# Kernel optimization log

Measured on AMD Instinct MI355X. Metric: run time of the kernel, lower is better.

Reference implementation:

```python
import jax, jax.numpy as jnp
import numpy as np

NPOINT, K = 1024, 16
BN_EPS = 1e-5


def farthest_point_sample(xyz, npoint):
    # xyz: [B, N, 3]. Deterministic start at index 0 (torch version uses randint).
    B, N, _ = xyz.shape

    def step(carry, _):
        distance, farthest = carry
        centroid = jnp.take_along_axis(xyz, farthest[:, None, None], axis=1)  # [B,1,3]
        dist = jnp.sum((xyz - centroid) ** 2, axis=-1)  # [B,N]
        distance = jnp.minimum(distance, dist)
        nxt = jnp.argmax(distance, axis=-1)
        return (distance, nxt), farthest

    init = (jnp.full((B, N), 1e10, dtype=xyz.dtype), jnp.zeros((B,), dtype=jnp.int32))
    _, cents = jax.lax.scan(step, init, None, length=npoint)
    return jnp.transpose(cents)  # [B, npoint]


def knn_idx(k, xyz, new_xyz):
    # squared distances [B,S,N] via ||a||^2 + ||b||^2 - 2 a.b (avoids [B,S,N,3] blowup)
    d = (jnp.sum(new_xyz ** 2, -1)[:, :, None]
         + jnp.sum(xyz ** 2, -1)[:, None, :]
         - 2.0 * jnp.einsum('bsc,bnc->bsn', new_xyz, xyz))
    _, idx = jax.lax.top_k(-d, k)  # k smallest distances
    return idx


def gather_points(points, idx):
    # points: [B,N,C], idx: [B,...] -> [B,...,C]
    return jax.vmap(lambda p, i: p[i])(points, idx)


def bn_train(x, gamma, beta):
    # BatchNorm1d in train mode: batch statistics, biased variance
    m = jnp.mean(x, axis=0)
    v = jnp.var(x, axis=0)
    return gamma * (x - m) * jax.lax.rsqrt(v + BN_EPS) + beta


def setup_inputs() -> dict:
    key = jax.random.key(0)
    ks = jax.random.split(key, 16)
    B, N, CIN, COUT = 8, 4096, 64, 128
    cin3 = CIN + 3          # 67
    ec = int(cin3 * 2.0)    # 134 (expand_ratio=2, hidden_ch arg is unused by InvResMLP)
    s = 0.05
    return {
        'xyz': jax.random.normal(ks[0], (B, N, 3), jnp.float32),
        'pts': jax.random.normal(ks[1], (B, N, CIN), jnp.float32),
        'fc1_w': jax.random.normal(ks[2], (cin3, ec), jnp.float32) * s,
        'fc1_b': jnp.zeros((ec,), jnp.float32),
        'bn1_g': jnp.ones((ec,), jnp.float32),
        'bn1_b': jnp.zeros((ec,), jnp.float32),
        'fc2_w': jax.random.normal(ks[3], (ec, ec), jnp.float32) * s,
        'fc2_b': jnp.zeros((ec,), jnp.float32),
        'bn2_g': jnp.ones((ec,), jnp.float32),
        'bn2_b': jnp.zeros((ec,), jnp.float32),
        'fc3_w': jax.random.normal(ks[4], (ec, COUT), jnp.float32) * s,
        'fc3_b': jnp.zeros((COUT,), jnp.float32),
        'bn3_g': jnp.ones((COUT,), jnp.float32),
        'bn3_b': jnp.zeros((COUT,), jnp.float32),
        'sc_w': jax.random.normal(ks[5], (cin3, COUT), jnp.float32) * s,
        'sc_b': jnp.zeros((COUT,), jnp.float32),
        'scbn_g': jnp.ones((COUT,), jnp.float32),
        'scbn_b': jnp.zeros((COUT,), jnp.float32),
    }


def reference(xyz, pts, fc1_w, fc1_b, bn1_g, bn1_b, fc2_w, fc2_b, bn2_g, bn2_b,
              fc3_w, fc3_b, bn3_g, bn3_b, sc_w, sc_b, scbn_g, scbn_b):
    # --- local_group: FPS + kNN grouping ---
    cent = farthest_point_sample(xyz, NPOINT)          # [B,S]
    new_xyz = gather_points(xyz, cent)                 # [B,S,3]
    idx = knn_idx(K, xyz, new_xyz)                     # [B,S,K]
    grouped_xyz = gather_points(xyz, idx)              # [B,S,K,3]
    grouped_pts = gather_points(pts, idx)              # [B,S,K,C]
    grouped_xyz_norm = grouped_xyz - new_xyz[:, :, None, :]
    x = jnp.concatenate([grouped_xyz_norm, grouped_pts], axis=-1)  # [B,S,K,C+3]

    # --- InvResMLP (pointwise, train-mode BN, dropout as identity) ---
    B, S, Kk, C = x.shape
    x = x.reshape(B * S * Kk, C)
    sc = bn_train(x @ sc_w + sc_b, scbn_g, scbn_b)
    h = jax.nn.relu(bn_train(x @ fc1_w + fc1_b, bn1_g, bn1_b))
    h = jax.nn.relu(bn_train(h @ fc2_w + fc2_b, bn2_g, bn2_b))
    h = bn_train(h @ fc3_w + fc3_b, bn3_g, bn3_b)
    h = jax.nn.relu(h + sc)
    feats = h.reshape(B, S, Kk, -1)

    new_pts = jnp.max(feats, axis=2)                   # [B,S,out_ch]
    return new_xyz, new_pts
```

## Files before the change

### kernel.cpp

```cpp
#include <hip/hip_runtime.h>
#include <cstdint>
#include <cstddef>

typedef short short8 __attribute__((ext_vector_type(8)));
typedef float f32x4 __attribute__((ext_vector_type(4)));

#define B_   8
#define N_   4096
#define S_   1024
#define K_   16
#define M_   131072
#define CIN_ 64

__device__ inline float bf2f(unsigned short u) {
    unsigned int v = ((unsigned int)u) << 16;
    return __builtin_bit_cast(float, v);
}
__device__ inline unsigned short f2bf(float f) {
    unsigned int u = __builtin_bit_cast(unsigned int, f);
    unsigned int lsb = (u >> 16) & 1u;
    u += 0x7fffu + lsb;
    return (unsigned short)(u >> 16);
}

template<int CTRL>
__device__ inline unsigned long long dpp_max(unsigned long long k) {
    unsigned lo = (unsigned)k, hi = (unsigned)(k >> 32);
    unsigned olo = (unsigned)__builtin_amdgcn_update_dpp(0, (int)lo, CTRL, 0xF, 0xF, true);
    unsigned ohi = (unsigned)__builtin_amdgcn_update_dpp(0, (int)hi, CTRL, 0xF, 0xF, true);
    unsigned long long ok = ((unsigned long long)ohi << 32) | (unsigned long long)olo;
    return ok > k ? ok : k;
}
__device__ inline unsigned long long swz16_max(unsigned long long k) {
    unsigned lo = (unsigned)k, hi = (unsigned)(k >> 32);
    unsigned olo = (unsigned)__builtin_amdgcn_ds_swizzle((int)lo, 0x401F);
    unsigned ohi = (unsigned)__builtin_amdgcn_ds_swizzle((int)hi, 0x401F);
    unsigned long long ok = ((unsigned long long)ohi << 32) | (unsigned long long)olo;
    return ok > k ? ok : k;
}
__device__ inline unsigned long long shf32_max(unsigned long long k) {
    unsigned lo = (unsigned)k, hi = (unsigned)(k >> 32);
    unsigned olo = (unsigned)__shfl_xor((int)lo, 32);
    unsigned ohi = (unsigned)__shfl_xor((int)hi, 32);
    unsigned long long ok = ((unsigned long long)ohi << 32) | (unsigned long long)olo;
    return ok > k ? ok : k;
}

__global__ __launch_bounds__(256) void fps_kernel(const float* __restrict__ xyz,
                                                  float* __restrict__ outxyz)
{
    __shared__ float px_s[N_], py_s[N_], pz_s[N_];
    __shared__ float sOut[S_ * 3];
    __shared__ unsigned long long sK[2][4];
    int b = blockIdx.x;
    const float* xb = xyz + (size_t)b * N_ * 3;
    int t = threadIdx.x;
    int w = t >> 6, l = t & 63;
    const int NP = 16;
    float px[NP], py[NP], pz[NP], dst[NP];
#pragma unroll
    for (int i = 0; i < NP; i++) {
        int p = i * 256 + t;
        px[i] = xb[p * 3 + 0];
        py[i] = xb[p * 3 + 1];
        pz[i] = xb[p * 3 + 2];
        dst[i] = 1e10f;
        px_s[p] = px[i]; py_s[p] = py[i]; pz_s[p] = pz[i];
        asm volatile("" : "+v"(px[i]), "+v"(py[i]), "+v"(pz[i]));
    }
    __syncthreads();
    float cx = px_s[0], cy = py_s[0], cz = pz_s[0];
    for (int s = 0; s < S_; s++) {
        if (t == 0) { sOut[s * 3 + 0] = cx; sOut[s * 3 + 1] = cy; sOut[s * 3 + 2] = cz; }
        if (s == S_ - 1) break;
        float bd = -1.0f; int bp = 0;
#pragma unroll
        for (int i = 0; i < NP; i++) {
            float dx = __fsub_rn(px[i], cx);
            float dy = __fsub_rn(py[i], cy);
            float dz = __fsub_rn(pz[i], cz);
            float d  = __fadd_rn(__fadd_rn(__fmul_rn(dx, dx), __fmul_rn(dy, dy)),
                                 __fmul_rn(dz, dz));
            float nd = fminf(dst[i], d);
            dst[i] = nd;
            if (nd > bd) { bd = nd; bp = i * 256 + t; }
        }
        unsigned long long key =
            ((unsigned long long)__builtin_bit_cast(unsigned, bd) << 32) |
            (unsigned long long)(unsigned)(4095 - bp);
        key = dpp_max<0xB1>(key);
        key = dpp_max<0x4E>(key);
        key = dpp_max<0x141>(key);
        key = dpp_max<0x140>(key);
        key = swz16_max(key);
        key = shf32_max(key);
        int par = s & 1;
        if (l == 0) sK[par][w] = key;
        __syncthreads();
        unsigned long long k0 = sK[par][0], k1 = sK[par][1];
        unsigned long long k2 = sK[par][2], k3 = sK[par][3];
        unsigned long long ka = k0 > k1 ? k0 : k1;
        unsigned long long kb = k2 > k3 ? k2 : k3;
        unsigned long long g  = ka > kb ? ka : kb;
        int p = 4095 - (int)(g & 0xFFFu);
        cx = px_s[p]; cy = py_s[p]; cz = pz_s[p];
    }
    __syncthreads();
    float* ob = outxyz + (size_t)b * S_ * 3;
    for (int i = t; i < S_ * 3; i += 256) ob[i] = sOut[i];
}

__global__ void sqn_kernel(const float* __restrict__ xyz, float* __restrict__ sqn)
{
    int i = blockIdx.x * 256 + threadIdx.x;
    if (i >= B_ * N_) return;
    float x = xyz[i * 3 + 0], y = xyz[i * 3 + 1], z = xyz[i * 3 + 2];
    sqn[i] = __fadd_rn(__fadd_rn(__fmul_rn(x, x), __fmul_rn(y, y)), __fmul_rn(z, z));
}

__global__ __launch_bounds__(256) void knn_kernel(const float* __restrict__ xyz,
                                                  const float* __restrict__ sqn,
                                                  const float* __restrict__ newxyz,
                                                  int* __restrict__ idx)
{
    int w = threadIdx.x >> 6, l = threadIdx.x & 63;
    int q = blockIdx.x * 4 + w;
    int b = q >> 10;
    const float* xb = xyz + (size_t)b * N_ * 3;
    const float* sb = sqn + (size_t)b * N_;
    float qx = newxyz[(size_t)q * 3 + 0];
    float qy = newxyz[(size_t)q * 3 + 1];
    float qz = newxyz[(size_t)q * 3 + 2];
    float sa = __fadd_rn(__fadd_rn(__fmul_rn(qx, qx), __fmul_rn(qy, qy)), __fmul_rn(qz, qz));

    float d16[16]; int i16[16];
#pragma unroll
    for (int j = 0; j < 16; j++) { d16[j] = 3.0e38f; i16[j] = -1; }
    for (int i = 0; i < N_ / 64; i++) {
        int n = i * 64 + l;
        float bx = xb[n * 3 + 0], by = xb[n * 3 + 1], bz = xb[n * 3 + 2];
        float dot = __fmaf_rn(qz, bz, __fmaf_rn(qy, by, __fmul_rn(qx, bx)));
        float d = __fsub_rn(__fadd_rn(sa, sb[n]), __fmul_rn(2.0f, dot));
        if (d < d16[0]) {
            d16[0] = d; i16[0] = n;
#pragma unroll
            for (int j = 0; j < 15; j++) {
                if (d16[j] < d16[j + 1]) {
                    float td = d16[j]; d16[j] = d16[j + 1]; d16[j + 1] = td;
                    int   ti = i16[j]; i16[j] = i16[j + 1]; i16[j + 1] = ti;
                }
            }
        }
    }
    int* iq = idx + (size_t)q * 16;
#pragma unroll
    for (int r = 0; r < 16; r++) {
        float cd = d16[15]; int cn = i16[15];
#pragma unroll
        for (int off = 1; off < 64; off <<= 1) {
            float od = __shfl_xor(cd, off);
            int   on = __shfl_xor(cn, off);
            if (od < cd || (od == cd && on < cn)) { cd = od; cn = on; }
        }
        if (l == 0) iq[r] = cn;
        if (i16[15] == cn) {
#pragma unroll
            for (int j = 15; j >= 1; j--) { d16[j] = d16[j - 1]; i16[j] = i16[j - 1]; }
            d16[0] = 3.0e38f; i16[0] = -1;
        }
    }
}

__global__ void build_x(const float* __restrict__ xyz, const float* __restrict__ pts,
                        const float* __restrict__ newxyz, const int* __restrict__ idx,
                        unsigned short* __restrict__ X)
{
    size_t tid = (size_t)blockIdx.x * 256 + threadIdx.x;
    if (tid >= (size_t)M_ * 96) return;
    int c = (int)(tid % 96);
    size_t r = tid / 96;
    int s = (int)((r >> 4) & 1023);
    int b = (int)(r >> 14);
    int n = idx[r];
    float v;
    if (c < 3)      v = xyz[((size_t)b * N_ + n) * 3 + c] - newxyz[((size_t)b * S_ + s) * 3 + c];
    else if (c < 67) v = pts[((size_t)b * N_ + n) * CIN_ + (c - 3)];
    else             v = 0.0f;
    X[tid] = f2bf(v);
}

__global__ void fill_wt(unsigned short* __restrict__ dst, const float* __restrict__ src,
                        int Kreal, int Nrows, int Nsrc, int KPAD)
{
    int tid = blockIdx.x * 256 + threadIdx.x;
    if (tid >= Nrows * KPAD) return;
    int row = tid / KPAD, k = tid % KPAD;
    float v = (k < Kreal && row < Nsrc) ? src[(size_t)k * Nsrc + row] : 0.0f;
    dst[tid] = f2bf(v);
}

template<int KPAD, int NF>
__global__ __launch_bounds__(256) void gemm_bn(
    const unsigned short* __restrict__ A, const unsigned short* __restrict__ Wt,
    unsigned short* __restrict__ Z1, int ld1, int n1real, float* sum1, float* sq1,
    unsigned short* __restrict__ Z2, int ld2, int n2real, float* sum2, float* sq2,
    int split)
{
    __shared__ unsigned short sA[128 * KPAD];
    __shared__ float sSt[NF * 32];
    int t = threadIdx.x;
    int r0 = blockIdx.x * 128;
    for (int i = t; i < NF * 32; i += 256) sSt[i] = 0.0f;
    {
        const uint4* ga = (const uint4*)(A + (size_t)r0 * KPAD);
        uint4* la = (uint4*)sA;
        const int CNT = 128 * KPAD * 2 / 16;
        for (int i = t; i < CNT; i += 256) la[i] = ga[i];
    }
    __syncthreads();
    int w = t >> 6, l = t & 63, lhi = l >> 4, llo = l & 15;
    f32x4 acc[2][NF];
#pragma unroll
    for (int m = 0; m < 2; m++)
#pragma unroll
        for (int n = 0; n < NF; n++) acc[m][n] = (f32x4){0.f, 0.f, 0.f, 0.f};
#pragma unroll
    for (int ks = 0; ks < KPAD / 32; ks++) {
        short8 bfr[NF];
#pragma unroll
        for (int n = 0; n < NF; n++)
            bfr[n] = *(const short8*)(Wt + (size_t)(n * 16 + llo) * KPAD + ks * 32 + lhi * 8);
#pragma unroll
        for (int m = 0; m < 2; m++) {
            short8 afr = *(const short8*)(sA + (w * 32 + m * 16 + llo) * KPAD + ks * 32 + lhi * 8);
#pragma unroll
            for (int n = 0; n < NF; n++)
                acc[m][n] = __builtin_amdgcn_mfma_f32_16x16x32_bf16(afr, bfr[n], acc[m][n], 0, 0, 0);
        }
    }
#pragma unroll
    for (int n = 0; n < NF; n++) {
        int c = n * 16 + llo;
        float ss = 0.f, sq = 0.f;
#pragma unroll
        for (int m = 0; m < 2; m++) {
#pragma unroll
            for (int j = 0; j < 4; j++) {
                float v = acc[m][n][j];
                int row = r0 + w * 32 + m * 16 + lhi * 4 + j;
                unsigned short hv = f2bf(v);
                if (c < split) Z1[(size_t)row * ld1 + c] = hv;
                else           Z2[(size_t)row * ld2 + (c - split)] = hv;
                ss += v; sq += v * v;
            }
        }
        ss += __shfl_xor(ss, 16); ss += __shfl_xor(ss, 32);
        sq += __shfl_xor(sq, 16); sq += __shfl_xor(sq, 32);
        if (l < 16) { atomicAdd(&sSt[c * 2], ss); atomicAdd(&sSt[c * 2 + 1], sq); }
    }
    __syncthreads();
    for (int c = t; c < NF * 16; c += 256) {
        float ss = sSt[c * 2], sq = sSt[c * 2 + 1];
        if (c < split) {
            if (c < n1real) { atomicAdd(&sum1[c], ss); atomicAdd(&sq1[c], sq); }
        } else {
            int cc = c - split;
            if (cc < n2real) { atomicAdd(&sum2[cc], ss); atomicAdd(&sq2[cc], sq); }
        }
    }
}

__global__ void bn_finalize(const float* __restrict__ sum, const float* __restrict__ sq,
                            const float* __restrict__ g, const float* __restrict__ bb,
                            float* __restrict__ a, float* __restrict__ c, int n)
{
    int i = blockIdx.x * 256 + threadIdx.x;
    if (i >= n) return;
    const float inv = 1.0f / (float)M_;
    float m = sum[i] * inv;
    float var = sq[i] * inv - m * m;
    float av = g[i] * rsqrtf(var + 1e-5f);
    a[i] = av;
    c[i] = bb[i] - av * m;
}

__global__ void norm_relu(const unsigned short* __restrict__ Z, int zld, int nreal,
                          unsigned short* __restrict__ H, int hld,
                          const float* __restrict__ a, const float* __restrict__ c,
                          size_t total)
{
    size_t tid = (size_t)blockIdx.x * 256 + threadIdx.x;
    if (tid >= total) return;
    int col = (int)(tid % hld);
    size_t r = tid / hld;
    float v = 0.0f;
    if (col < nreal) v = fmaxf(a[col] * bf2f(Z[r * zld + col]) + c[col], 0.0f);
    H[r * hld + col] = f2bf(v);
}

__global__ void final_kernel(const unsigned short* __restrict__ Z3,
                             const unsigned short* __restrict__ ZSC,
                             const float* __restrict__ a3, const float* __restrict__ c3,
                             const float* __restrict__ asc, const float* __restrict__ csc,
                             float* __restrict__ out)
{
    int tid = blockIdx.x * 256 + threadIdx.x;
    int ch = tid & 127, bs = tid >> 7;
    float A3 = a3[ch], C3 = c3[ch], AS = asc[ch], CS = csc[ch];
    float mx = 0.0f;
    for (int k = 0; k < 16; k++) {
        size_t row = (size_t)bs * 16 + k;
        float v3 = bf2f(Z3[row * 128 + ch]);
        float vs = bf2f(ZSC[row * 128 + ch]);
        float y = fmaxf(A3 * v3 + C3 + AS * vs + CS, 0.0f);
        mx = fmaxf(mx, y);
    }
    out[24576 + (size_t)bs * 128 + ch] = mx;
}

#define WS_STATS 0
#define WS_WT1   16384
#define WS_WT2   68608
#define WS_WT3   114688
#define WS_SQN   155648
#define WS_IDX   286720
#define WS_X     811008
#define WS_Z     25976832
#define WS_ZSC   63725568
#define WS_H     97280000

extern "C" void kernel_launch(void* const* d_in, const int* in_sizes, int n_in,
                              void* d_out, int out_size, void* d_ws, size_t ws_size,
                              hipStream_t stream)
{
    const float* xyz    = (const float*)d_in[0];
    const float* pts    = (const float*)d_in[1];
    const float* fc1_w  = (const float*)d_in[2];
    const float* bn1_g  = (const float*)d_in[4];
    const float* bn1_b  = (const float*)d_in[5];
    const float* fc2_w  = (const float*)d_in[6];
    const float* bn2_g  = (const float*)d_in[8];
    const float* bn2_b  = (const float*)d_in[9];
    const float* fc3_w  = (const float*)d_in[10];
    const float* bn3_g  = (const float*)d_in[12];
    const float* bn3_b  = (const float*)d_in[13];
    const float* sc_w   = (const float*)d_in[14];
    const float* scbn_g = (const float*)d_in[16];
    const float* scbn_b = (const float*)d_in[17];

    char* ws = (char*)d_ws;
    float* st = (float*)(ws + WS_STATS);
    float* bn1_sum = st + 0,    *bn1_sq = st + 134;
    float* bnsc_sum = st + 268, *bnsc_sq = st + 396;
    float* bn2_sum = st + 524,  *bn2_sq = st + 658;
    float* bn3_sum = st + 792,  *bn3_sq = st + 920;
    float* a1 = st + 1048, *c1 = st + 1182;
    float* a2 = st + 1316, *c2 = st + 1450;
    float* a3 = st + 1584, *c3 = st + 1712;
    float* asc = st + 1840, *csc = st + 1968;

    unsigned short* WT1 = (unsigned short*)(ws + WS_WT1);
    unsigned short* WT2 = (unsigned short*)(ws + WS_WT2);
    unsigned short* WT3 = (unsigned short*)(ws + WS_WT3);
    float* SQN = (float*)(ws + WS_SQN);
    int*   IDX = (int*)(ws + WS_IDX);
    unsigned short* X   = (unsigned short*)(ws + WS_X);
    unsigned short* Z   = (unsigned short*)(ws + WS_Z);
    unsigned short* ZSC = (unsigned short*)(ws + WS_ZSC);
    unsigned short* H   = (unsigned short*)(ws + WS_H);
    float* out = (float*)d_out;

    hipMemsetAsync(ws + WS_STATS, 0, 1048 * 4, stream);

    fill_wt<<<54, 256, 0, stream>>>(WT1, fc1_w, 67, 144, 134, 96);
    fill_wt<<<48, 256, 0, stream>>>(WT1 + 144 * 96, sc_w, 67, 128, 128, 96);
    fill_wt<<<90, 256, 0, stream>>>(WT2, fc2_w, 134, 144, 134, 160);
    fill_wt<<<80, 256, 0, stream>>>(WT3, fc3_w, 134, 128, 128, 160);

    fps_kernel<<<8, 256, 0, stream>>>(xyz, out);
    sqn_kernel<<<128, 256, 0, stream>>>(xyz, SQN);
    knn_kernel<<<2048, 256, 0, stream>>>(xyz, SQN, out, IDX);
    build_x<<<49152, 256, 0, stream>>>(xyz, pts, out, IDX, X);

    gemm_bn<96, 17><<<1024, 256, 0, stream>>>(X, WT1,
        Z, 144, 134, bn1_sum, bn1_sq,
        ZSC, 128, 128, bnsc_sum, bnsc_sq, 144);
    bn_finalize<<<1, 256, 0, stream>>>(bn1_sum, bn1_sq, bn1_g, bn1_b, a1, c1, 134);
    bn_finalize<<<1, 256, 0, stream>>>(bnsc_sum, bnsc_sq, scbn_g, scbn_b, asc, csc, 128);
    norm_relu<<<81920, 256, 0, stream>>>(Z, 144, 134, H, 160, a1, c1, (size_t)M_ * 160);

    gemm_bn<160, 9><<<1024, 256, 0, stream>>>(H, WT2,
        Z, 144, 134, bn2_sum, bn2_sq,
        Z, 144, 0, bn2_sum, bn2_sq, 144);
    bn_finalize<<<1, 256, 0, stream>>>(bn2_sum, bn2_sq, bn2_g, bn2_b, a2, c2, 134);
    norm_relu<<<81920, 256, 0, stream>>>(Z, 144, 134, H, 160, a2, c2, (size_t)M_ * 160);

    gemm_bn<160, 8><<<1024, 256, 0, stream>>>(H, WT3,
        Z, 128, 128, bn3_sum, bn3_sq,
        Z, 128, 0, bn3_sum, bn3_sq, 128);
    bn_finalize<<<1, 256, 0, stream>>>(bn3_sum, bn3_sq, bn3_g, bn3_b, a3, c3, 128);

    final_kernel<<<4096, 256, 0, stream>>>(Z, ZSC, a3, c3, asc, csc, out);
}
```

Baseline: 1.139 ms.

## Vectorize elementwise kernels and use DPP broadcast for the FPS wave reduction

Replaces the ds_swizzle and shfl_xor stages of the FPS argmax reduction with DPP row_bcast15 and row_bcast31 steps, and reads the result from lane 63. Rewrites build_x, norm_relu and final_kernel so each thread handles 8–16 contiguous bf16 elements with 128-bit short8 loads and stores, instead of one scalar element per thread with div/mod indexing. The grids shrink to match. The goal is to cut per-element index arithmetic and narrow memory transactions in these bandwidth-bound passes, at the cost of more registers per thread. norm_relu_v reads the scale and shift arrays slightly past the real channel count before masking those values.

New measurement: 1.124 ms. No clear change (-1.4%).

```diff
diff --git a/kernel.cpp b/kernel.cpp
--- a/kernel.cpp
+++ b/kernel.cpp
@@ -28,20 +28,6 @@
     unsigned lo = (unsigned)k, hi = (unsigned)(k >> 32);
     unsigned olo = (unsigned)__builtin_amdgcn_update_dpp(0, (int)lo, CTRL, 0xF, 0xF, true);
     unsigned ohi = (unsigned)__builtin_amdgcn_update_dpp(0, (int)hi, CTRL, 0xF, 0xF, true);
-    unsigned long long ok = ((unsigned long long)ohi << 32) | (unsigned long long)olo;
-    return ok > k ? ok : k;
-}
-__device__ inline unsigned long long swz16_max(unsigned long long k) {
-    unsigned lo = (unsigned)k, hi = (unsigned)(k >> 32);
-    unsigned olo = (unsigned)__builtin_amdgcn_ds_swizzle((int)lo, 0x401F);
-    unsigned ohi = (unsigned)__builtin_amdgcn_ds_swizzle((int)hi, 0x401F);
-    unsigned long long ok = ((unsigned long long)ohi << 32) | (unsigned long long)olo;
-    return ok > k ? ok : k;
-}
-__device__ inline unsigned long long shf32_max(unsigned long long k) {
-    unsigned lo = (unsigned)k, hi = (unsigned)(k >> 32);
-    unsigned olo = (unsigned)__shfl_xor((int)lo, 32);
-    unsigned ohi = (unsigned)__shfl_xor((int)hi, 32);
     unsigned long long ok = ((unsigned long long)ohi << 32) | (unsigned long long)olo;
     return ok > k ? ok : k;
 }
@@ -92,10 +78,10 @@
         key = dpp_max<0x4E>(key);
         key = dpp_max<0x141>(key);
         key = dpp_max<0x140>(key);
-        key = swz16_max(key);
-        key = shf32_max(key);
+        key = dpp_max<0x142>(key);
+        key = dpp_max<0x143>(key);
         int par = s & 1;
-        if (l == 0) sK[par][w] = key;
+        if (l == 63) sK[par][w] = key;
         __syncthreads();
         unsigned long long k0 = sK[par][0], k1 = sK[par][1];
         unsigned long long k2 = sK[par][2], k3 = sK[par][3];
@@ -175,18 +161,38 @@
                         const float* __restrict__ newxyz, const int* __restrict__ idx,
                         unsigned short* __restrict__ X)
 {
-    size_t tid = (size_t)blockIdx.x * 256 + threadIdx.x;
-    if (tid >= (size_t)M_ * 96) return;
-    int c = (int)(tid % 96);
-    size_t r = tid / 96;
-    int s = (int)((r >> 4) & 1023);
-    int b = (int)(r >> 14);
-    int n = idx[r];
-    float v;
-    if (c < 3)      v = xyz[((size_t)b * N_ + n) * 3 + c] - newxyz[((size_t)b * S_ + s) * 3 + c];
-    else if (c < 67) v = pts[((size_t)b * N_ + n) * CIN_ + (c - 3)];
-    else             v = 0.0f;
-    X[tid] = f2bf(v);
+    int tid = blockIdx.x * 256 + threadIdx.x;
+    int j = tid % 6;
+    int r = tid / 6;
+    float v[16];
+#pragma unroll
+    for (int e = 0; e < 16; e++) v[e] = 0.0f;
+    if (j < 5) {
+        int n = idx[r];
+        int s = (r >> 4) & 1023;
+        int b = r >> 14;
+        const float* pr = pts + ((size_t)b * N_ + n) * CIN_;
+        if (j == 0) {
+#pragma unroll
+            for (int c = 0; c < 3; c++)
+                v[c] = xyz[((size_t)b * N_ + n) * 3 + c] - newxyz[((size_t)b * S_ + s) * 3 + c];
+#pragma unroll
+            for (int c = 3; c < 16; c++) v[c] = pr[c - 3];
+        } else if (j == 4) {
+#pragma unroll
+            for (int c = 0; c < 3; c++) v[c] = pr[61 + c];
+        } else {
+            int base = j * 16 - 3;
+#pragma unroll
+            for (int c = 0; c < 16; c++) v[c] = pr[base + c];
+        }
+    }
+    short8 lo, hi;
+#pragma unroll
+    for (int e = 0; e < 8; e++) { lo[e] = (short)f2bf(v[e]); hi[e] = (short)f2bf(v[8 + e]); }
+    unsigned short* xp = X + (size_t)r * 96 + j * 16;
+    *(short8*)xp = lo;
+    *(short8*)(xp + 8) = hi;
 }
 
 __global__ void fill_wt(unsigned short* __restrict__ dst, const float* __restrict__ src,
@@ -284,18 +290,26 @@
     c[i] = bb[i] - av * m;
 }
 
-__global__ void norm_relu(const unsigned short* __restrict__ Z, int zld, int nreal,
-                          unsigned short* __restrict__ H, int hld,
-                          const float* __restrict__ a, const float* __restrict__ c,
-                          size_t total)
-{
-    size_t tid = (size_t)blockIdx.x * 256 + threadIdx.x;
-    if (tid >= total) return;
-    int col = (int)(tid % hld);
-    size_t r = tid / hld;
-    float v = 0.0f;
-    if (col < nreal) v = fmaxf(a[col] * bf2f(Z[r * zld + col]) + c[col], 0.0f);
-    H[r * hld + col] = f2bf(v);
+__global__ void norm_relu_v(const unsigned short* __restrict__ Z,
+                            unsigned short* __restrict__ H,
+                            const float* __restrict__ a, const float* __restrict__ c)
+{
+    int tid = blockIdx.x * 256 + threadIdx.x;
+    int j = tid % 20;
+    size_t r = (size_t)(tid / 20);
+    int col0 = j * 8;
+    short8 hv = {0, 0, 0, 0, 0, 0, 0, 0};
+    if (col0 < 134) {
+        short8 zv = *(const short8*)(Z + r * 144 + col0);
+#pragma unroll
+        for (int e = 0; e < 8; e++) {
+            int col = col0 + e;
+            float av = a[col], cv = c[col];
+            float v = fmaxf(av * bf2f((unsigned short)zv[e]) + cv, 0.0f);
+            hv[e] = (col < 134) ? (short)f2bf(v) : (short)0;
+        }
+    }
+    *(short8*)(H + r * 160 + col0) = hv;
 }
 
 __global__ void final_kernel(const unsigned short* __restrict__ Z3,
@@ -305,17 +319,30 @@
                              float* __restrict__ out)
 {
     int tid = blockIdx.x * 256 + threadIdx.x;
-    int ch = tid & 127, bs = tid >> 7;
-    float A3 = a3[ch], C3 = c3[ch], AS = asc[ch], CS = csc[ch];
-    float mx = 0.0f;
+    int bs = tid >> 4, ch0 = (tid & 15) * 8;
+    float A3[8], C3[8], AS[8], CS[8], mx[8];
+#pragma unroll
+    for (int e = 0; e < 8; e++) {
+        A3[e] = a3[ch0 + e]; C3[e] = c3[ch0 + e];
+        AS[e] = asc[ch0 + e]; CS[e] = csc[ch0 + e];
+        mx[e] = 0.0f;
+    }
+    const unsigned short* z3p = Z3 + (size_t)bs * 16 * 128 + ch0;
+    const unsigned short* zsp = ZSC + (size_t)bs * 16 * 128 + ch0;
+#pragma unroll
     for (int k = 0; k < 16; k++) {
-        size_t row = (size_t)bs * 16 + k;
-        float v3 = bf2f(Z3[row * 128 + ch]);
-        float vs = bf2f(ZSC[row * 128 + ch]);
-        float y = fmaxf(A3 * v3 + C3 + AS * vs + CS, 0.0f);
-        mx = fmaxf(mx, y);
-    }
-    out[24576 + (size_t)bs * 128 + ch] = mx;
+        short8 z3 = *(const short8*)(z3p + (size_t)k * 128);
+        short8 zs = *(const short8*)(zsp + (size_t)k * 128);
+#pragma unroll
+        for (int e = 0; e < 8; e++) {
+            float y = fmaxf(A3[e] * bf2f((unsigned short)z3[e]) + C3[e]
+                            + AS[e] * bf2f((unsigned short)zs[e]) + CS[e], 0.0f);
+            mx[e] = fmaxf(mx[e], y);
+        }
+    }
+    float* op = out + 24576 + (size_t)bs * 128 + ch0;
+#pragma unroll
+    for (int e = 0; e < 8; e++) op[e] = mx[e];
 }
 
 #define WS_STATS 0
@@ -380,25 +407,25 @@
     fps_kernel<<<8, 256, 0, stream>>>(xyz, out);
     sqn_kernel<<<128, 256, 0, stream>>>(xyz, SQN);
     knn_kernel<<<2048, 256, 0, stream>>>(xyz, SQN, out, IDX);
-    build_x<<<49152, 256, 0, stream>>>(xyz, pts, out, IDX, X);
+    build_x<<<3072, 256, 0, stream>>>(xyz, pts, out, IDX, X);
 
     gemm_bn<96, 17><<<1024, 256, 0, stream>>>(X, WT1,
         Z, 144, 134, bn1_sum, bn1_sq,
         ZSC, 128, 128, bnsc_sum, bnsc_sq, 144);
     bn_finalize<<<1, 256, 0, stream>>>(bn1_sum, bn1_sq, bn1_g, bn1_b, a1, c1, 134);
     bn_finalize<<<1, 256, 0, stream>>>(bnsc_sum, bnsc_sq, scbn_g, scbn_b, asc, csc, 128);
-    norm_relu<<<81920, 256, 0, stream>>>(Z, 144, 134, H, 160, a1, c1, (size_t)M_ * 160);
+    norm_relu_v<<<10240, 256, 0, stream>>>(Z, H, a1, c1);
 
     gemm_bn<160, 9><<<1024, 256, 0, stream>>>(H, WT2,
         Z, 144, 134, bn2_sum, bn2_sq,
         Z, 144, 0, bn2_sum, bn2_sq, 144);
     bn_finalize<<<1, 256, 0, stream>>>(bn2_sum, bn2_sq, bn2_g, bn2_b, a2, c2, 134);
-    norm_relu<<<81920, 256, 0, stream>>>(Z, 144, 134, H, 160, a2, c2, (size_t)M_ * 160);
+    norm_relu_v<<<10240, 256, 0, stream>>>(Z, H, a2, c2);
 
     gemm_bn<160, 8><<<1024, 256, 0, stream>>>(H, WT3,
         Z, 128, 128, bn3_sum, bn3_sq,
         Z, 128, 0, bn3_sum, bn3_sq, 128);
     bn_finalize<<<1, 256, 0, stream>>>(bn3_sum, bn3_sq, bn3_g, bn3_b, a3, c3, 128);
 
-    final_kernel<<<4096, 256, 0, stream>>>(Z, ZSC, a3, c3, asc, csc, out);
-}
+    final_kernel<<<512, 256, 0, stream>>>(Z, ZSC, a3, c3, asc, csc, out);
+}
```
